# Kernel tuning notes

Hardware: AMD Instinct MI355X
Metric: run time of the kernel (lower is better)

Reference implementation:

```python
import jax, jax.numpy as jnp
import numpy as np

K = 4096  # num_embeddings
D = 256   # embedding_dim

def setup_inputs() -> dict:
    key = jax.random.key(0)
    k1, k2 = jax.random.split(key)
    z_e = jax.random.normal(k1, (32, 32, 32, 256), dtype=jnp.float32)
    embedding = jax.random.normal(k2, (K, D), dtype=jnp.float32)
    return {"z_e": z_e, "embedding": embedding}

def reference(z_e, embedding):
    # z_e: [B,H,W,D] channels-last; embedding: [K,D]
    B, H, W, Dd = z_e.shape
    z_flat = z_e.reshape(-1, Dd)                                   # [N,D]
    # squared L2 distances via expansion: ||z||^2 + ||e||^2 - 2 z.e
    distances = (jnp.sum(z_flat**2, axis=1, keepdims=True)
                 + jnp.sum(embedding**2, axis=1)
                 - 2.0 * jnp.matmul(z_flat, embedding.T))          # [N,K]
    indices = jnp.argmin(distances, axis=1)                        # [N]
    z_q = embedding[indices].reshape(B, H, W, Dd)                  # gather
    # straight-through estimator
    z_q = z_e + jax.lax.stop_gradient(z_q - z_e)
    # perplexity (codebook utilization)
    avg_probs = jnp.bincount(indices, length=K).astype(jnp.float32) / indices.shape[0]
    perplexity = jnp.exp(-jnp.sum(avg_probs * jnp.log(avg_probs + 1e-10)))
    return z_q, indices.reshape(B, H, W), perplexity
```

## Files before the change

kernel.cpp:

```cpp
#include <hip/hip_runtime.h>
#include <hip/hip_bf16.h>
#include <math.h>
#include <stdint.h>

typedef _Float16 f16;
typedef _Float16 f16x8 __attribute__((ext_vector_type(8)));
typedef float f32x16 __attribute__((ext_vector_type(16)));

#define DIM 256
#define LOSCALE 2048.0f
#define INV_LOSCALE (1.0f/2048.0f)

#define BP_BYTES (4096u*1024u + 98304u)

#define GLOAD16(gp, lp) __builtin_amdgcn_global_load_lds( \
    (const __attribute__((address_space(1))) void*)(gp),  \
    (__attribute__((address_space(3))) void*)(lp), 16, 0, 0)

__global__ void vq_pack2(const float* __restrict__ emb, f16* __restrict__ bp)
{
    int o = blockIdx.x * blockDim.x + threadIdx.x;
    int l = o & 63;
    int b = o >> 6;
    int t   = b & 1;
    int s   = (b >> 1) & 15;
    int col = b >> 5;
    int code  = col * 32 + (l & 31);
    int depth = s * 16 + (l >> 5) * 8;
    const float* gp = emb + (size_t)code * DIM + depth;
    float4 x0 = *(const float4*)gp;
    float4 x1 = *(const float4*)(gp + 4);
    float xs[8] = {x0.x, x0.y, x0.z, x0.w, x1.x, x1.y, x1.z, x1.w};
    f16x8 v;
    #pragma unroll
    for (int j = 0; j < 8; ++j) {
        f16 h = (f16)xs[j];
        v[j] = t ? (f16)((xs[j] - (float)h) * LOSCALE) : h;
    }
    *(f16x8*)(bp + (size_t)o * 8) = v;
}

__global__ void vq_e2(const float* __restrict__ emb, float* __restrict__ e2) {
    int k = blockIdx.x;
    int l = threadIdx.x;
    float4 v = ((const float4*)(emb + (size_t)k * DIM))[l];
    float s = v.x * v.x + v.y * v.y + v.z * v.z + v.w * v.w;
    #pragma unroll
    for (int off = 32; off; off >>= 1) s += __shfl_xor(s, off);
    if (l == 0) e2[k] = s;
}

__global__ void vq_zero(int* __restrict__ p, int n) {
    int i = blockIdx.x * blockDim.x + threadIdx.x;
    if (i < n) p[i] = 0;
}

__global__ __launch_bounds__(512, 2) void vq_argmin9(
    const float* __restrict__ z, const char* __restrict__ bp,
    const float* __restrict__ e2, unsigned long long* __restrict__ part)
{
    __shared__ __align__(16) char bufs[4][32768];
    __shared__ float e2s[2048];

    const int t    = threadIdx.x;
    const int lane = t & 63;
    const int wv   = t >> 6;
    const int hw   = blockIdx.x & 1;
    const int rg   = blockIdx.x >> 1;
    const int l31  = lane & 31;
    const int hi5  = lane >> 5;
    const int rowbase = rg * 256 + wv * 32;

    *(float4*)&e2s[t * 4] = *(const float4*)(e2 + hw * 2048 + t * 4);

    f16x8 a_h[16], a_l[16];
    {
        const float* zr = z + (size_t)(rowbase + l31) * DIM + hi5 * 8;
        #pragma unroll
        for (int s = 0; s < 16; ++s) {
            float4 x0 = *(const float4*)(zr + s * 16);
            float4 x1 = *(const float4*)(zr + s * 16 + 4);
            float xs[8] = {x0.x, x0.y, x0.z, x0.w, x1.x, x1.y, x1.z, x1.w};
            #pragma unroll
            for (int j = 0; j < 8; ++j) {
                f16 h = (f16)xs[j];
                a_h[s][j] = h;
                a_l[s][j] = (f16)((xs[j] - (float)h) * LOSCALE);
            }
        }
    }

    const char* bhalf = bp + ((size_t)hw << 21);

#define STAGE(pb, cc) do {                                                    \
    const char* src_ = bhalf + ((size_t)(cc) << 15) + (size_t)t * 16;         \
    char* dst_ = bufs[pb] + t * 16;                                           \
    _Pragma("unroll")                                                         \
    for (int i_ = 0; i_ < 4; ++i_)                                            \
        GLOAD16(src_ + i_ * 8192, dst_ + i_ * 8192);                          \
    } while (0)

    STAGE(0, 0);
    STAGE(1, 1);
    __syncthreads();

    float    bestd[16];
    unsigned bcol[4];
    #pragma unroll
    for (int q = 0; q < 16; ++q) bestd[q] = 3.4e38f;
    #pragma unroll
    for (int i = 0; i < 4; ++i) bcol[i] = 0u;

    for (int c = 0; c < 64; ++c) {
        STAGE((c + 2) & 3, c + 2);

        asm volatile("s_waitcnt vmcnt(8)" ::: "memory");
        asm volatile("s_waitcnt lgkmcnt(0)" ::: "memory");
        __builtin_amdgcn_s_barrier();
        __builtin_amdgcn_sched_barrier(0);

        f32x16 acc0, acc1a, acc1b;
        #pragma unroll
        for (int q = 0; q < 16; ++q) { acc0[q] = 0.0f; acc1a[q] = 0.0f; acc1b[q] = 0.0f; }

        const char* bb = bufs[c & 3];
        f16x8 bh_ = *(const f16x8*)(bb + lane * 16);
        f16x8 bl_ = *(const f16x8*)(bb + 1024 + lane * 16);
        __builtin_amdgcn_s_setprio(1);
        #pragma unroll
        for (int ks = 0; ks < 16; ++ks) {
            f16x8 bhn_, bln_;
            if (ks < 15) {
                bhn_ = *(const f16x8*)(bb + (ks + 1) * 2048 + lane * 16);
                bln_ = *(const f16x8*)(bb + (ks + 1) * 2048 + 1024 + lane * 16);
            }
            acc0  = __builtin_amdgcn_mfma_f32_32x32x16_f16(a_h[ks], bh_, acc0,  0, 0, 0);
            acc1a = __builtin_amdgcn_mfma_f32_32x32x16_f16(a_h[ks], bl_, acc1a, 0, 0, 0);
            acc1b = __builtin_amdgcn_mfma_f32_32x32x16_f16(a_l[ks], bh_, acc1b, 0, 0, 0);
            if (ks < 15) { bh_ = bhn_; bl_ = bln_; }
        }
        __builtin_amdgcn_s_setprio(0);

        float e2c = e2s[c * 32 + l31];
        #pragma unroll
        for (int q = 0; q < 16; ++q) {
            float dot  = fmaf(acc1a[q] + acc1b[q], INV_LOSCALE, acc0[q]);
            float dist = fmaf(-2.0f, dot, e2c);
            bool  lt   = dist < bestd[q];
            bestd[q]   = lt ? dist : bestd[q];
            const unsigned sh = (unsigned)((q & 3) * 8);
            unsigned nv = (bcol[q >> 2] & ~(0xFFu << sh)) | ((unsigned)c << sh);
            bcol[q >> 2] = lt ? nv : bcol[q >> 2];
        }
    }
#undef STAGE

    #pragma unroll
    for (int q = 0; q < 16; ++q) {
        float    d = bestd[q];
        unsigned c = (unsigned)(hw * 2048) +
                     ((bcol[q >> 2] >> ((q & 3) * 8)) & 0xFFu) * 32u + (unsigned)l31;
        #pragma unroll
        for (int o2 = 16; o2; o2 >>= 1) {
            float    od = __shfl_xor(d, o2);
            unsigned oc = __shfl_xor(c, o2);
            if (od < d || (od == d && oc < c)) { d = od; c = oc; }
        }
        if (l31 == 0) {
            int row = (q & 3) + 8 * (q >> 2) + 4 * hi5;
            unsigned u   = __float_as_uint(d);
            unsigned key = u ^ (unsigned)(((int)u >> 31) | 0x80000000);
            part[(size_t)hw * 32768 + rowbase + row] =
                ((unsigned long long)key << 32) | c;
        }
    }
}

__global__ void vq_final(const unsigned long long* __restrict__ part,
                         const float* __restrict__ emb,
                         float* __restrict__ idxf, float* __restrict__ zq,
                         int* __restrict__ counts, int N)
{
    int n = blockIdx.x * 4 + (threadIdx.x >> 6);
    int l = threadIdx.x & 63;
    if (n >= N) return;
    unsigned long long a = part[n];
    unsigned long long b = part[(size_t)N + n];
    unsigned long long m = b < a ? b : a;
    int idx = (int)(unsigned)(m & 0xffffffffu);
    ((float4*)(zq + (size_t)n * DIM))[l] =
        ((const float4*)(emb + (size_t)idx * DIM))[l];
    if (l == 0) {
        idxf[n] = (float)idx;
        atomicAdd(&counts[idx], 1);
    }
}

__global__ __launch_bounds__(256, 2) void vq_argmin_f32(
    const float* __restrict__ z, const float* __restrict__ emb,
    const float* __restrict__ e2, float* __restrict__ idxf, int K)
{
    __shared__ float zs[64 * 36];
    __shared__ float es[128 * 36];
    const int t = threadIdx.x;
    const int tx = t & 15;
    const int ty = t >> 4;
    const int rowbase = blockIdx.x * 64;
    const float* zbase = z + (size_t)rowbase * DIM;
    float best[4]; int bidx[4];
    #pragma unroll
    for (int i = 0; i < 4; ++i) { best[i] = 3.4e38f; bidx[i] = 0; }
    for (int kt = 0; kt < K; kt += 128) {
        float acc[4][8];
        #pragma unroll
        for (int i = 0; i < 4; ++i)
            #pragma unroll
            for (int j = 0; j < 8; ++j) acc[i][j] = 0.0f;
        for (int dc = 0; dc < DIM; dc += 32) {
            { int lr = t >> 2, o = (t & 3) * 8;
              const float* gp = zbase + (size_t)lr * DIM + dc + o;
              *(float4*)&zs[lr*36+o]   = *(const float4*)gp;
              *(float4*)&zs[lr*36+o+4] = *(const float4*)(gp+4); }
            { int lc = t >> 1, o = (t & 1) * 16;
              const float* gp = emb + (size_t)(kt+lc) * DIM + dc + o;
              *(float4*)&es[lc*36+o]    = *(const float4*)gp;
              *(float4*)&es[lc*36+o+4]  = *(const float4*)(gp+4);
              *(float4*)&es[lc*36+o+8]  = *(const float4*)(gp+8);
              *(float4*)&es[lc*36+o+12] = *(const float4*)(gp+12); }
            __syncthreads();
            const float* zp = &zs[(ty*4)*36];
            const float* ep = &es[tx*36];
            #pragma unroll
            for (int d = 0; d < 32; d += 4) {
                float4 zv[4], ev[8];
                #pragma unroll
                for (int i = 0; i < 4; ++i) zv[i] = *(const float4*)&zp[i*36+d];
                #pragma unroll
                for (int j = 0; j < 8; ++j) ev[j] = *(const float4*)&ep[j*16*36+d];
                #pragma unroll
                for (int i = 0; i < 4; ++i)
                    #pragma unroll
                    for (int j = 0; j < 8; ++j) {
                        acc[i][j] += zv[i].x*ev[j].x; acc[i][j] += zv[i].y*ev[j].y;
                        acc[i][j] += zv[i].z*ev[j].z; acc[i][j] += zv[i].w*ev[j].w;
                    }
            }
            __syncthreads();
        }
        #pragma unroll
        for (int j = 0; j < 8; ++j) {
            int c = kt + tx + 16*j;
            float ev2 = e2[c];
            #pragma unroll
            for (int i = 0; i < 4; ++i) {
                float dist = ev2 - 2.0f*acc[i][j];
                if (dist < best[i] || (dist == best[i] && c < bidx[i])) { best[i]=dist; bidx[i]=c; }
            }
        }
    }
    #pragma unroll
    for (int i = 0; i < 4; ++i) {
        float bd = best[i]; int bi = bidx[i];
        #pragma unroll
        for (int off = 8; off; off >>= 1) {
            float od = __shfl_xor(bd, off); int oi = __shfl_xor(bi, off);
            if (od < bd || (od == bd && oi < bi)) { bd = od; bi = oi; }
        }
        if (tx == 0) idxf[rowbase + ty*4 + i] = (float)bi;
    }
}

__global__ void vq_gather(const float* __restrict__ emb,
                          const float* __restrict__ idxf,
                          float* __restrict__ zq, int N)
{
    int n = blockIdx.x * 4 + (threadIdx.x >> 6);
    int l = threadIdx.x & 63;
    if (n >= N) return;
    int idx = (int)idxf[n];
    ((float4*)(zq + (size_t)n * DIM))[l] = ((const float4*)(emb + (size_t)idx * DIM))[l];
}

__global__ void vq_hist(const float* __restrict__ idxf, int* __restrict__ counts, int N) {
    int n = blockIdx.x * blockDim.x + threadIdx.x;
    if (n < N) atomicAdd(&counts[(int)idxf[n]], 1);
}

__global__ void vq_ppl(const int* __restrict__ counts, float invN,
                       float* __restrict__ out, int K)
{
    int t = threadIdx.x;
    float s = 0.0f;
    for (int k = t; k < K; k += 256) {
        float p = (float)counts[k] * invN;
        s += p * logf(p + 1e-10f);
    }
    #pragma unroll
    for (int off = 32; off; off >>= 1) s += __shfl_xor(s, off);
    __shared__ float wsum[4];
    if ((t & 63) == 0) wsum[t >> 6] = s;
    __syncthreads();
    if (t == 0) out[0] = expf(-(wsum[0] + wsum[1] + wsum[2] + wsum[3]));
}

extern "C" void kernel_launch(void* const* d_in, const int* in_sizes, int n_in,
                              void* d_out, int out_size, void* d_ws, size_t ws_size,
                              hipStream_t stream)
{
    const float* z   = (const float*)d_in[0];
    const float* emb = (const float*)d_in[1];
    const int N = in_sizes[0] / DIM;
    const int K = in_sizes[1] / DIM;

    float* out  = (float*)d_out;
    float* zq   = out;
    float* idxf = out + (size_t)N * DIM;
    float* ppl  = idxf + N;

    const size_t PART_BYTES = 2ull * 32768 * sizeof(unsigned long long);
    const size_t NEED = (size_t)BP_BYTES + 16384 + 16384 + PART_BYTES;

    if (ws_size >= NEED && K == 4096 && N == 32768) {
        f16*   bpk    = (f16*)d_ws;
        float* e2     = (float*)((char*)d_ws + BP_BYTES);
        int*   counts = (int*)((char*)d_ws + BP_BYTES + 16384);
        unsigned long long* part =
            (unsigned long long*)((char*)d_ws + BP_BYTES + 32768);

        vq_pack2<<<1024, 256, 0, stream>>>(emb, bpk);
        vq_e2<<<K, 64, 0, stream>>>(emb, e2);
        vq_zero<<<(K + 255) / 256, 256, 0, stream>>>(counts, K);
        vq_argmin9<<<(N / 256) * 2, 512, 0, stream>>>(z, (const char*)bpk, e2, part);
        vq_final<<<N / 4, 256, 0, stream>>>(part, emb, idxf, zq, counts, N);
        vq_ppl<<<1, 256, 0, stream>>>(counts, 1.0f / (float)N, ppl, K);
    } else {
        float* e2     = (float*)d_ws;
        int*   counts = (int*)((char*)d_ws + (size_t)K * sizeof(float));
        vq_e2<<<K, 64, 0, stream>>>(emb, e2);
        vq_zero<<<(K + 255) / 256, 256, 0, stream>>>(counts, K);
        vq_argmin_f32<<<N / 64, 256, 0, stream>>>(z, emb, e2, idxf, K);
        vq_gather<<<N / 4, 256, 0, stream>>>(emb, idxf, zq, N);
        vq_hist<<<(N + 255) / 256, 256, 0, stream>>>(idxf, counts, N);
        vq_ppl<<<1, 256, 0, stream>>>(counts, 1.0f / (float)N, ppl, K);
    }
}
```

Baseline: 223.5 us.

## Stage only hi codebook halves in LDS, stream lo halves from global

The argmin kernel now copies only the high-precision f16 codebook fragments into LDS, halving each staging buffer to 16 KB. The low-residual fragments are loaded straight from global memory into registers. The MFMA loop is restructured into four groups of four k-steps with register double-buffering of both fragment types. This cuts LDS traffic and footprint, which may allow more resident blocks per CU. The cost is that every wave redundantly fetches the lo fragments through the cache hierarchy, and the MFMAs now depend on global load latency.

```diff
diff --git a/kernel.cpp b/kernel.cpp
--- a/kernel.cpp
+++ b/kernel.cpp
@@ -55,11 +55,11 @@
     if (i < n) p[i] = 0;
 }
 
-__global__ __launch_bounds__(512, 2) void vq_argmin9(
+__global__ __launch_bounds__(512, 2) void vq_argmin11(
     const float* __restrict__ z, const char* __restrict__ bp,
     const float* __restrict__ e2, unsigned long long* __restrict__ part)
 {
-    __shared__ __align__(16) char bufs[4][32768];
+    __shared__ __align__(16) char bufs[4][16384];
     __shared__ float e2s[2048];
 
     const int t    = threadIdx.x;
@@ -93,12 +93,34 @@
     const char* bhalf = bp + ((size_t)hw << 21);
 
 #define STAGE(pb, cc) do {                                                    \
-    const char* src_ = bhalf + ((size_t)(cc) << 15) + (size_t)t * 16;         \
-    char* dst_ = bufs[pb] + t * 16;                                           \
+    const char* src_ = bhalf + ((size_t)(cc) << 15)                           \
+                     + (size_t)wv * 2048 + (size_t)lane * 16;                 \
+    char* dst_ = bufs[pb] + wv * 1024 + lane * 16;                            \
+    GLOAD16(src_, dst_);                                                      \
+    GLOAD16(src_ + 16384, dst_ + 8192);                                       \
+    } while (0)
+
+#define LOADBL(dst, CB, G) do {                                               \
     _Pragma("unroll")                                                         \
-    for (int i_ = 0; i_ < 4; ++i_)                                            \
-        GLOAD16(src_ + i_ * 8192, dst_ + i_ * 8192);                          \
+    for (int j_ = 0; j_ < 4; ++j_)                                            \
+        dst[j_] = *(const f16x8*)((CB) + ((G) * 4 + j_) * 2048 + 1024         \
+                                  + lane * 16);                               \
     } while (0)
+
+#define LOADBH(dst, BB, G) do {                                               \
+    _Pragma("unroll")                                                         \
+    for (int j_ = 0; j_ < 4; ++j_)                                            \
+        dst[j_] = *(const f16x8*)((BB) + ((G) * 4 + j_) * 1024 + lane * 16);  \
+    } while (0)
+
+#define MFMA4(BH, BL, G) do {                                                 \
+    _Pragma("unroll")                                                         \
+    for (int j_ = 0; j_ < 4; ++j_) {                                          \
+        const int ks_ = (G) * 4 + j_;                                         \
+        acc0  = __builtin_amdgcn_mfma_f32_32x32x16_f16(a_h[ks_], BH[j_], acc0,  0,0,0); \
+        acc1a = __builtin_amdgcn_mfma_f32_32x32x16_f16(a_h[ks_], BL[j_], acc1a, 0,0,0); \
+        acc1b = __builtin_amdgcn_mfma_f32_32x32x16_f16(a_l[ks_], BH[j_], acc1b, 0,0,0); \
+    } } while (0)
 
     STAGE(0, 0);
     STAGE(1, 1);
@@ -112,6 +134,10 @@
     for (int i = 0; i < 4; ++i) bcol[i] = 0u;
 
     for (int c = 0; c < 64; ++c) {
+        const char* colbase = bhalf + ((size_t)c << 15);
+
+        f16x8 blA[4], blB[4];
+        LOADBL(blA, colbase, 0);
         STAGE((c + 2) & 3, c + 2);
 
         asm volatile("s_waitcnt vmcnt(8)" ::: "memory");
@@ -124,21 +150,20 @@
         for (int q = 0; q < 16; ++q) { acc0[q] = 0.0f; acc1a[q] = 0.0f; acc1b[q] = 0.0f; }
 
         const char* bb = bufs[c & 3];
-        f16x8 bh_ = *(const f16x8*)(bb + lane * 16);
-        f16x8 bl_ = *(const f16x8*)(bb + 1024 + lane * 16);
+        f16x8 bhA[4], bhB[4];
+        LOADBH(bhA, bb, 0);
+
         __builtin_amdgcn_s_setprio(1);
-        #pragma unroll
-        for (int ks = 0; ks < 16; ++ks) {
-            f16x8 bhn_, bln_;
-            if (ks < 15) {
-                bhn_ = *(const f16x8*)(bb + (ks + 1) * 2048 + lane * 16);
-                bln_ = *(const f16x8*)(bb + (ks + 1) * 2048 + 1024 + lane * 16);
-            }
-            acc0  = __builtin_amdgcn_mfma_f32_32x32x16_f16(a_h[ks], bh_, acc0,  0, 0, 0);
-            acc1a = __builtin_amdgcn_mfma_f32_32x32x16_f16(a_h[ks], bl_, acc1a, 0, 0, 0);
-            acc1b = __builtin_amdgcn_mfma_f32_32x32x16_f16(a_l[ks], bh_, acc1b, 0, 0, 0);
-            if (ks < 15) { bh_ = bhn_; bl_ = bln_; }
-        }
+        LOADBL(blB, colbase, 1);
+        LOADBH(bhB, bb, 1);
+        MFMA4(bhA, blA, 0);
+        LOADBL(blA, colbase, 2);
+        LOADBH(bhA, bb, 2);
+        MFMA4(bhB, blB, 1);
+        LOADBL(blB, colbase, 3);
+        LOADBH(bhB, bb, 3);
+        MFMA4(bhA, blA, 2);
+        MFMA4(bhB, blB, 3);
         __builtin_amdgcn_s_setprio(0);
 
         float e2c = e2s[c * 32 + l31];
@@ -154,6 +179,9 @@
         }
     }
 #undef STAGE
+#undef LOADBL
+#undef LOADBH
+#undef MFMA4
 
     #pragma unroll
     for (int q = 0; q < 16; ++q) {
@@ -330,7 +358,7 @@
         vq_pack2<<<1024, 256, 0, stream>>>(emb, bpk);
         vq_e2<<<K, 64, 0, stream>>>(emb, e2);
         vq_zero<<<(K + 255) / 256, 256, 0, stream>>>(counts, K);
-        vq_argmin9<<<(N / 256) * 2, 512, 0, stream>>>(z, (const char*)bpk, e2, part);
+        vq_argmin11<<<(N / 256) * 2, 512, 0, stream>>>(z, (const char*)bpk, e2, part);
         vq_final<<<N / 4, 256, 0, stream>>>(part, emb, idxf, zq, counts, N);
         vq_ppl<<<1, 256, 0, stream>>>(counts, 1.0f / (float)N, ppl, K);
     } else {
```

After: 235.0 us. 1.05x slower.

## Split argmin chunk loop into four barrier-synchronized phases interleaving loads and MFMA

Applied to the files above, without the earlier changes.

Restructures the per-chunk inner loop into four phases, each issuing one quarter of the next-next chunk's global-to-LDS load, reading four k-slices of B into registers, then running a block of MFMAs between workgroup barriers. The goal is to spread memory issue across the chunk and to batch LDS reads ahead of the MFMA bursts so waves stay in lockstep. It adds eight barriers per chunk instead of one, which could cost more synchronization stall than the overlap it gains.

```diff
diff --git a/kernel.cpp b/kernel.cpp
--- a/kernel.cpp
+++ b/kernel.cpp
@@ -55,7 +55,7 @@
     if (i < n) p[i] = 0;
 }
 
-__global__ __launch_bounds__(512, 2) void vq_argmin9(
+__global__ __launch_bounds__(512, 2) void vq_argmin12(
     const float* __restrict__ z, const char* __restrict__ bp,
     const float* __restrict__ e2, unsigned long long* __restrict__ part)
 {
@@ -92,7 +92,7 @@
 
     const char* bhalf = bp + ((size_t)hw << 21);
 
-#define STAGE(pb, cc) do {                                                    \
+#define STAGEF(pb, cc) do {                                                   \
     const char* src_ = bhalf + ((size_t)(cc) << 15) + (size_t)t * 16;         \
     char* dst_ = bufs[pb] + t * 16;                                           \
     _Pragma("unroll")                                                         \
@@ -100,8 +100,40 @@
         GLOAD16(src_ + i_ * 8192, dst_ + i_ * 8192);                          \
     } while (0)
 
-    STAGE(0, 0);
-    STAGE(1, 1);
+#define STAGE1(pb, cc, g) do {                                                \
+    const char* src_ = bhalf + ((size_t)(cc) << 15) + (size_t)t * 16          \
+                     + (size_t)(g) * 8192;                                    \
+    char* dst_ = bufs[pb] + t * 16 + (g) * 8192;                              \
+    GLOAD16(src_, dst_);                                                      \
+    } while (0)
+
+#define PHASE(g) do {                                                         \
+    STAGE1((c + 2) & 3, c + 2, g);                                            \
+    if ((g) == 0) asm volatile("s_waitcnt vmcnt(5)" ::: "memory");            \
+    _Pragma("unroll")                                                         \
+    for (int j_ = 0; j_ < 4; ++j_) {                                          \
+        rh[j_] = *(const f16x8*)(bb + ((g) * 4 + j_) * 2048 + lane * 16);     \
+        rl[j_] = *(const f16x8*)(bb + ((g) * 4 + j_) * 2048 + 1024 + lane * 16); \
+    }                                                                         \
+    __builtin_amdgcn_sched_barrier(0);                                        \
+    __builtin_amdgcn_s_barrier();                                             \
+    asm volatile("s_waitcnt lgkmcnt(0)" ::: "memory");                        \
+    __builtin_amdgcn_sched_barrier(0);                                        \
+    __builtin_amdgcn_s_setprio(1);                                            \
+    _Pragma("unroll")                                                         \
+    for (int j_ = 0; j_ < 4; ++j_) {                                          \
+        const int ks_ = (g) * 4 + j_;                                         \
+        acc0  = __builtin_amdgcn_mfma_f32_32x32x16_f16(a_h[ks_], rh[j_], acc0,  0,0,0); \
+        acc1a = __builtin_amdgcn_mfma_f32_32x32x16_f16(a_h[ks_], rl[j_], acc1a, 0,0,0); \
+        acc1b = __builtin_amdgcn_mfma_f32_32x32x16_f16(a_l[ks_], rh[j_], acc1b, 0,0,0); \
+    }                                                                         \
+    __builtin_amdgcn_s_setprio(0);                                            \
+    __builtin_amdgcn_sched_barrier(0);                                        \
+    __builtin_amdgcn_s_barrier();                                             \
+    } while (0)
+
+    STAGEF(0, 0);
+    STAGEF(1, 1);
     __syncthreads();
 
     float    bestd[16];
@@ -112,34 +144,16 @@
     for (int i = 0; i < 4; ++i) bcol[i] = 0u;
 
     for (int c = 0; c < 64; ++c) {
-        STAGE((c + 2) & 3, c + 2);
-
-        asm volatile("s_waitcnt vmcnt(8)" ::: "memory");
-        asm volatile("s_waitcnt lgkmcnt(0)" ::: "memory");
-        __builtin_amdgcn_s_barrier();
-        __builtin_amdgcn_sched_barrier(0);
-
+        const char* bb = bufs[c & 3];
         f32x16 acc0, acc1a, acc1b;
         #pragma unroll
         for (int q = 0; q < 16; ++q) { acc0[q] = 0.0f; acc1a[q] = 0.0f; acc1b[q] = 0.0f; }
 
-        const char* bb = bufs[c & 3];
-        f16x8 bh_ = *(const f16x8*)(bb + lane * 16);
-        f16x8 bl_ = *(const f16x8*)(bb + 1024 + lane * 16);
-        __builtin_amdgcn_s_setprio(1);
-        #pragma unroll
-        for (int ks = 0; ks < 16; ++ks) {
-            f16x8 bhn_, bln_;
-            if (ks < 15) {
-                bhn_ = *(const f16x8*)(bb + (ks + 1) * 2048 + lane * 16);
-                bln_ = *(const f16x8*)(bb + (ks + 1) * 2048 + 1024 + lane * 16);
-            }
-            acc0  = __builtin_amdgcn_mfma_f32_32x32x16_f16(a_h[ks], bh_, acc0,  0, 0, 0);
-            acc1a = __builtin_amdgcn_mfma_f32_32x32x16_f16(a_h[ks], bl_, acc1a, 0, 0, 0);
-            acc1b = __builtin_amdgcn_mfma_f32_32x32x16_f16(a_l[ks], bh_, acc1b, 0, 0, 0);
-            if (ks < 15) { bh_ = bhn_; bl_ = bln_; }
-        }
-        __builtin_amdgcn_s_setprio(0);
+        f16x8 rh[4], rl[4];
+        PHASE(0);
+        PHASE(1);
+        PHASE(2);
+        PHASE(3);
 
         float e2c = e2s[c * 32 + l31];
         #pragma unroll
@@ -153,7 +167,9 @@
             bcol[q >> 2] = lt ? nv : bcol[q >> 2];
         }
     }
-#undef STAGE
+#undef STAGEF
+#undef STAGE1
+#undef PHASE
 
     #pragma unroll
     for (int q = 0; q < 16; ++q) {
@@ -330,7 +346,7 @@
         vq_pack2<<<1024, 256, 0, stream>>>(emb, bpk);
         vq_e2<<<K, 64, 0, stream>>>(emb, e2);
         vq_zero<<<(K + 255) / 256, 256, 0, stream>>>(counts, K);
-        vq_argmin9<<<(N / 256) * 2, 512, 0, stream>>>(z, (const char*)bpk, e2, part);
+        vq_argmin12<<<(N / 256) * 2, 512, 0, stream>>>(z, (const char*)bpk, e2, part);
         vq_final<<<N / 4, 256, 0, stream>>>(part, emb, idxf, zq, counts, N);
         vq_ppl<<<1, 256, 0, stream>>>(counts, 1.0f / (float)N, ppl, K);
     } else {
```

Measured after the change: 235.5 us. 1.05x slower.

## Scan with fp16-only dot products and rescore ambiguous rows at split precision

Applied to the files above, without the earlier changes.

The main argmin scan now uses a single fp16 MFMA product per tile instead of three split-precision products, and it tracks both the best and second-best distance per row. A certification kernel uses error bounds built from row norms and the largest codebook residual norms to accept rows whose best-versus-second margin is safe. The remaining rows go to a compacted list and are rescored with the full hi/lo split-precision MFMA over the whole codebook, merged by atomicMin. This cuts MFMA work in the main pass by about a factor of three, at the cost of extra kernels, atomics and a rescore pass whose size depends on how many rows are ambiguous. Correctness depends on the error bound being conservative.

```diff
diff --git a/kernel.cpp b/kernel.cpp
--- a/kernel.cpp
+++ b/kernel.cpp
@@ -6,16 +6,23 @@
 typedef _Float16 f16;
 typedef _Float16 f16x8 __attribute__((ext_vector_type(8)));
 typedef float f32x16 __attribute__((ext_vector_type(16)));
+typedef unsigned long long ull;
 
 #define DIM 256
 #define LOSCALE 2048.0f
 #define INV_LOSCALE (1.0f/2048.0f)
+#define EPS0 0.05f
 
 #define BP_BYTES (4096u*1024u + 98304u)
 
 #define GLOAD16(gp, lp) __builtin_amdgcn_global_load_lds( \
     (const __attribute__((address_space(1))) void*)(gp),  \
     (__attribute__((address_space(3))) void*)(lp), 16, 0, 0)
+
+__device__ __forceinline__ float dec_key(unsigned k) {
+    unsigned u = (k & 0x80000000u) ? (k ^ 0x80000000u) : ~k;
+    return __uint_as_float(u);
+}
 
 __global__ void vq_pack2(const float* __restrict__ emb, f16* __restrict__ bp)
 {
@@ -40,11 +47,42 @@
     *(f16x8*)(bp + (size_t)o * 8) = v;
 }
 
+__global__ void vq_e2x(const float* __restrict__ emb, float* __restrict__ e2,
+                       unsigned* __restrict__ melmeh)
+{
+    int k = blockIdx.x;
+    int l = threadIdx.x;
+    float4 v = ((const float4*)(emb + (size_t)k * DIM))[l];
+    float xs[4] = {v.x, v.y, v.z, v.w};
+    float s = 0.0f, sh = 0.0f, sl = 0.0f;
+    #pragma unroll
+    for (int j = 0; j < 4; ++j) {
+        float x = xs[j];
+        s = fmaf(x, x, s);
+        f16 h = (f16)x;
+        float hv = (float)h;
+        float lv = (float)((f16)((x - hv) * LOSCALE));
+        sh = fmaf(hv, hv, sh);
+        sl = fmaf(lv, lv, sl);
+    }
+    #pragma unroll
+    for (int off = 32; off; off >>= 1) {
+        s  += __shfl_xor(s, off);
+        sh += __shfl_xor(sh, off);
+        sl += __shfl_xor(sl, off);
+    }
+    if (l == 0) {
+        e2[k] = s;
+        atomicMax(&melmeh[0], __float_as_uint(sqrtf(sl)));
+        atomicMax(&melmeh[1], __float_as_uint(sqrtf(sh)));
+    }
+}
+
 __global__ void vq_e2(const float* __restrict__ emb, float* __restrict__ e2) {
     int k = blockIdx.x;
     int l = threadIdx.x;
     float4 v = ((const float4*)(emb + (size_t)k * DIM))[l];
-    float s = v.x * v.x + v.y * v.y + v.z * v.z + v.w * v.w;
+    float s = v.x*v.x + v.y*v.y + v.z*v.z + v.w*v.w;
     #pragma unroll
     for (int off = 32; off; off >>= 1) s += __shfl_xor(s, off);
     if (l == 0) e2[k] = s;
@@ -55,9 +93,11 @@
     if (i < n) p[i] = 0;
 }
 
-__global__ __launch_bounds__(512, 2) void vq_argmin9(
+__global__ __launch_bounds__(512, 2) void vq_scan(
     const float* __restrict__ z, const char* __restrict__ bp,
-    const float* __restrict__ e2, unsigned long long* __restrict__ part)
+    const float* __restrict__ e2,
+    ull* __restrict__ partD, float* __restrict__ partD2,
+    float2* __restrict__ AB)
 {
     __shared__ __align__(16) char bufs[4][32768];
     __shared__ float e2s[2048];
@@ -73,7 +113,8 @@
 
     *(float4*)&e2s[t * 4] = *(const float4*)(e2 + hw * 2048 + t * 4);
 
-    f16x8 a_h[16], a_l[16];
+    f16x8 a_h[16];
+    float s2h = 0.0f, s2l = 0.0f;
     {
         const float* zr = z + (size_t)(rowbase + l31) * DIM + hi5 * 8;
         #pragma unroll
@@ -85,13 +126,301 @@
             for (int j = 0; j < 8; ++j) {
                 f16 h = (f16)xs[j];
                 a_h[s][j] = h;
+                float hv = (float)h;
+                float lv = (float)((f16)((xs[j] - hv) * LOSCALE));
+                s2h = fmaf(hv, hv, s2h);
+                s2l = fmaf(lv, lv, s2l);
+            }
+        }
+    }
+    s2h += __shfl_xor(s2h, 32);
+    s2l += __shfl_xor(s2l, 32);
+    if (hw == 0 && lane < 32) {
+        float nzh = sqrtf(s2h), nzl = sqrtf(s2l);
+        float a = (2.0f / LOSCALE) * (nzh + nzl * INV_LOSCALE) * 1.02f;
+        float b = (2.0f / LOSCALE) * nzl * 1.02f;
+        AB[rowbase + lane] = make_float2(a, b);
+    }
+
+    const char* bhalf = bp + ((size_t)hw << 21);
+
+#define STAGE(pb, uu) do {                                                    \
+    const char* s0_ = bhalf + ((size_t)(uu) << 16)                            \
+                    + (size_t)(t >> 6) * 2048 + (size_t)(t & 63) * 16;        \
+    char* d0_ = bufs[pb] + t * 16;                                            \
+    GLOAD16(s0_,          d0_);                                               \
+    GLOAD16(s0_ + 16384,  d0_ + 8192);                                        \
+    GLOAD16(s0_ + 32768,  d0_ + 16384);                                       \
+    GLOAD16(s0_ + 49152,  d0_ + 24576);                                       \
+    } while (0)
+
+    STAGE(0, 0);
+    STAGE(1, 1);
+    __syncthreads();
+
+    float    bestd[16], d2nd[16];
+    unsigned bcol[4];
+    #pragma unroll
+    for (int q = 0; q < 16; ++q) { bestd[q] = 3.4e38f; d2nd[q] = 3.4e38f; }
+    #pragma unroll
+    for (int i = 0; i < 4; ++i) bcol[i] = 0u;
+
+    for (int u = 0; u < 32; ++u) {
+        STAGE((u + 2) & 3, u + 2);
+        asm volatile("s_waitcnt vmcnt(8)" ::: "memory");
+        asm volatile("s_waitcnt lgkmcnt(0)" ::: "memory");
+        __builtin_amdgcn_s_barrier();
+        __builtin_amdgcn_sched_barrier(0);
+
+        const char* bu = bufs[u & 3];
+        #pragma unroll
+        for (int sub = 0; sub < 2; ++sub) {
+            const int c = 2 * u + sub;
+            const char* bb = bu + sub * 16384;
+            f32x16 m0, m1;
+            #pragma unroll
+            for (int q = 0; q < 16; ++q) { m0[q] = 0.0f; m1[q] = 0.0f; }
+            __builtin_amdgcn_s_setprio(1);
+            #pragma unroll
+            for (int ks = 0; ks < 16; ks += 2) {
+                f16x8 b0 = *(const f16x8*)(bb + ks * 1024 + lane * 16);
+                f16x8 b1 = *(const f16x8*)(bb + (ks + 1) * 1024 + lane * 16);
+                m0 = __builtin_amdgcn_mfma_f32_32x32x16_f16(a_h[ks],     b0, m0, 0, 0, 0);
+                m1 = __builtin_amdgcn_mfma_f32_32x32x16_f16(a_h[ks + 1], b1, m1, 0, 0, 0);
+            }
+            __builtin_amdgcn_s_setprio(0);
+
+            float e2c = e2s[c * 32 + l31];
+            #pragma unroll
+            for (int q = 0; q < 16; ++q) {
+                float d = fmaf(-2.0f, m0[q] + m1[q], e2c);
+                bool lt = d < bestd[q];
+                float nd2 = lt ? bestd[q] : fminf(d2nd[q], d);
+                d2nd[q]  = nd2;
+                bestd[q] = lt ? d : bestd[q];
+                const unsigned sh = (unsigned)((q & 3) * 8);
+                unsigned nv = (bcol[q >> 2] & ~(0xFFu << sh)) | ((unsigned)c << sh);
+                bcol[q >> 2] = lt ? nv : bcol[q >> 2];
+            }
+        }
+    }
+#undef STAGE
+
+    #pragma unroll
+    for (int q = 0; q < 16; ++q) {
+        float    d  = bestd[q];
+        float    d2 = d2nd[q];
+        unsigned c  = (unsigned)(hw * 2048) +
+                      ((bcol[q >> 2] >> ((q & 3) * 8)) & 0xFFu) * 32u + (unsigned)l31;
+        #pragma unroll
+        for (int o2 = 16; o2; o2 >>= 1) {
+            float    od  = __shfl_xor(d, o2);
+            unsigned oc  = __shfl_xor(c, o2);
+            float    od2 = __shfl_xor(d2, o2);
+            float nd2 = fminf(fmaxf(d, od), fminf(d2, od2));
+            bool sw = od < d || (od == d && oc < c);
+            d = sw ? od : d;
+            c = sw ? oc : c;
+            d2 = nd2;
+        }
+        if (l31 == 0) {
+            int row = (q & 3) + 8 * (q >> 2) + 4 * hi5;
+            unsigned u_  = __float_as_uint(d);
+            unsigned key = u_ ^ (unsigned)(((int)u_ >> 31) | 0x80000000);
+            partD [(size_t)hw * 32768 + rowbase + row] = ((ull)key << 32) | c;
+            partD2[(size_t)hw * 32768 + rowbase + row] = d2;
+        }
+    }
+}
+
+__global__ void vq_certain(ull* __restrict__ partD, const float* __restrict__ partD2,
+                           const float2* __restrict__ AB,
+                           const unsigned* __restrict__ melmeh,
+                           int* __restrict__ list, int* __restrict__ ctr, int N)
+{
+    int i = blockIdx.x * blockDim.x + threadIdx.x;
+    if (i >= N) return;
+    ull k0 = partD[i];
+    ull k1 = partD[(size_t)N + i];
+    float d1a = dec_key((unsigned)(k0 >> 32));
+    float d1b = dec_key((unsigned)(k1 >> 32));
+    float d2a = partD2[i];
+    float d2b = partD2[(size_t)N + i];
+    ull  kmin = k1 < k0 ? k1 : k0;
+    float gd1 = fminf(d1a, d1b);
+    float gd2 = fminf(fmaxf(d1a, d1b), fminf(d2a, d2b));
+    float2 ab = AB[i];
+    float Mel = __uint_as_float(melmeh[0]);
+    float Meh = __uint_as_float(melmeh[1]);
+    float eps = fmaf(ab.x, Mel, fmaf(ab.y, Meh, EPS0));
+    if (gd2 - gd1 > 2.0f * eps) {
+        partD[i] = kmin;
+    } else {
+        partD[i] = ~0ULL;
+        int p = atomicAdd(ctr, 1);
+        list[p] = i;
+    }
+}
+
+__global__ __launch_bounds__(64) void vq_rescore(
+    const float* __restrict__ z, const char* __restrict__ bp,
+    const float* __restrict__ e2, const int* __restrict__ list,
+    const int* __restrict__ ctr, ull* __restrict__ outD)
+{
+    const int l    = threadIdx.x;
+    const int l31  = l & 31;
+    const int hi5  = l >> 5;
+    const int slot  = blockIdx.x >> 2;
+    const int chunk = blockIdx.x & 3;
+    const int cnt = *ctr;
+    if (slot * 32 >= cnt) return;
+
+    int pos = slot * 32 + l31;
+    int rid = list[pos < cnt ? pos : 0];
+
+    f16x8 a_h[16], a_l[16];
+    {
+        const float* zr = z + (size_t)rid * DIM + hi5 * 8;
+        #pragma unroll
+        for (int s = 0; s < 16; ++s) {
+            float4 x0 = *(const float4*)(zr + s * 16);
+            float4 x1 = *(const float4*)(zr + s * 16 + 4);
+            float xs[8] = {x0.x, x0.y, x0.z, x0.w, x1.x, x1.y, x1.z, x1.w};
+            #pragma unroll
+            for (int j = 0; j < 8; ++j) {
+                f16 h = (f16)xs[j];
+                a_h[s][j] = h;
                 a_l[s][j] = (f16)((xs[j] - (float)h) * LOSCALE);
             }
         }
     }
 
+    float    bestd[16];
+    unsigned bcol[4];
+    #pragma unroll
+    for (int q = 0; q < 16; ++q) bestd[q] = 3.4e38f;
+    #pragma unroll
+    for (int i = 0; i < 4; ++i) bcol[i] = 0u;
+
+    const char* bgp = bp + (((size_t)chunk * 32) << 15) + (size_t)l * 16;
+
+#define LOADG(BH, BL, OFF) do {                                    \
+    _Pragma("unroll")                                              \
+    for (int i_ = 0; i_ < 4; ++i_) {                               \
+        BH[i_] = *(const f16x8*)(bgp + (OFF) + i_ * 2048);         \
+        BL[i_] = *(const f16x8*)(bgp + (OFF) + i_ * 2048 + 1024);  \
+    } } while (0)
+
+#define COMPUTE(BH, BL, G) do {                                                      \
+    _Pragma("unroll")                                                                \
+    for (int i_ = 0; i_ < 4; ++i_) {                                                 \
+        acc0  = __builtin_amdgcn_mfma_f32_32x32x16_f16(a_h[(G)*4+i_], BH[i_], acc0,  0,0,0); \
+        acc1a = __builtin_amdgcn_mfma_f32_32x32x16_f16(a_h[(G)*4+i_], BL[i_], acc1a, 0,0,0); \
+        acc1b = __builtin_amdgcn_mfma_f32_32x32x16_f16(a_l[(G)*4+i_], BH[i_], acc1b, 0,0,0); \
+    } } while (0)
+
+    f16x8 h0[4], l0[4], h1[4], l1[4];
+    size_t off = 0;
+    LOADG(h0, l0, off); off += 8192;
+    LOADG(h1, l1, off); off += 8192;
+
+    for (int lc = 0; lc < 32; ++lc) {
+        float e2c = e2[(chunk * 32 + lc) * 32 + l31];
+        f32x16 acc0, acc1a, acc1b;
+        #pragma unroll
+        for (int q = 0; q < 16; ++q) { acc0[q] = 0.0f; acc1a[q] = 0.0f; acc1b[q] = 0.0f; }
+
+        COMPUTE(h0, l0, 0); LOADG(h0, l0, off); off += 8192;
+        COMPUTE(h1, l1, 1); LOADG(h1, l1, off); off += 8192;
+        COMPUTE(h0, l0, 2); LOADG(h0, l0, off); off += 8192;
+        COMPUTE(h1, l1, 3); LOADG(h1, l1, off); off += 8192;
+
+        #pragma unroll
+        for (int q = 0; q < 16; ++q) {
+            float dot  = fmaf(acc1a[q] + acc1b[q], INV_LOSCALE, acc0[q]);
+            float dist = fmaf(-2.0f, dot, e2c);
+            bool  lt   = dist < bestd[q];
+            bestd[q]   = lt ? dist : bestd[q];
+            const unsigned sh = (unsigned)((q & 3) * 8);
+            unsigned nv = (bcol[q >> 2] & ~(0xFFu << sh)) | ((unsigned)lc << sh);
+            bcol[q >> 2] = lt ? nv : bcol[q >> 2];
+        }
+    }
+#undef LOADG
+#undef COMPUTE
+
+    #pragma unroll
+    for (int q = 0; q < 16; ++q) {
+        float    d = bestd[q];
+        unsigned c = ((unsigned)chunk * 32u +
+                      ((bcol[q >> 2] >> ((q & 3) * 8)) & 0xFFu)) * 32u + (unsigned)l31;
+        #pragma unroll
+        for (int o2 = 16; o2; o2 >>= 1) {
+            float    od = __shfl_xor(d, o2);
+            unsigned oc = __shfl_xor(c, o2);
+            if (od < d || (od == d && oc < c)) { d = od; c = oc; }
+        }
+        int rlocal = (q & 3) + 8 * (q >> 2) + 4 * hi5;
+        int ridr   = __shfl(rid, rlocal);
+        if (l31 == 0) {
+            unsigned u_  = __float_as_uint(d);
+            unsigned key = u_ ^ (unsigned)(((int)u_ >> 31) | 0x80000000);
+            atomicMin(&outD[ridr], ((ull)key << 32) | c);
+        }
+    }
+}
+
+__global__ void vq_final1(const ull* __restrict__ outD, const float* __restrict__ emb,
+                          float* __restrict__ idxf, float* __restrict__ zq,
+                          int* __restrict__ counts, int N)
+{
+    int n = blockIdx.x * 4 + (threadIdx.x >> 6);
+    int l = threadIdx.x & 63;
+    if (n >= N) return;
+    int idx = (int)(unsigned)(outD[n] & 0xffffffffu);
+    idx &= 4095;
+    ((float4*)(zq + (size_t)n * DIM))[l] =
+        ((const float4*)(emb + (size_t)idx * DIM))[l];
+    if (l == 0) {
+        idxf[n] = (float)idx;
+        atomicAdd(&counts[idx], 1);
+    }
+}
+
+__global__ __launch_bounds__(512, 2) void vq_argmin10(
+    const float* __restrict__ z, const char* __restrict__ bp,
+    const float* __restrict__ e2, ull* __restrict__ part)
+{
+    __shared__ __align__(16) char bufs[4][32768];
+    __shared__ float e2s[2048];
+    const int t    = threadIdx.x;
+    const int lane = t & 63;
+    const int wv   = t >> 6;
+    const int hw   = blockIdx.x & 1;
+    const int rg   = blockIdx.x >> 1;
+    const int l31  = lane & 31;
+    const int hi5  = lane >> 5;
+    const int rowbase = rg * 256 + wv * 32;
+
+    *(float4*)&e2s[t * 4] = *(const float4*)(e2 + hw * 2048 + t * 4);
+
+    f16x8 a_h[16], a_l[16];
+    {
+        const float* zr = z + (size_t)(rowbase + l31) * DIM + hi5 * 8;
+        #pragma unroll
+        for (int s = 0; s < 16; ++s) {
+            float4 x0 = *(const float4*)(zr + s * 16);
+            float4 x1 = *(const float4*)(zr + s * 16 + 4);
+            float xs[8] = {x0.x, x0.y, x0.z, x0.w, x1.x, x1.y, x1.z, x1.w};
+            #pragma unroll
+            for (int j = 0; j < 8; ++j) {
+                f16 h = (f16)xs[j];
+                a_h[s][j] = h;
+                a_l[s][j] = (f16)((xs[j] - (float)h) * LOSCALE);
+            }
+        }
+    }
     const char* bhalf = bp + ((size_t)hw << 21);
-
 #define STAGE(pb, cc) do {                                                    \
     const char* src_ = bhalf + ((size_t)(cc) << 15) + (size_t)t * 16;         \
     char* dst_ = bufs[pb] + t * 16;                                           \
@@ -99,7 +428,6 @@
     for (int i_ = 0; i_ < 4; ++i_)                                            \
         GLOAD16(src_ + i_ * 8192, dst_ + i_ * 8192);                          \
     } while (0)
-
     STAGE(0, 0);
     STAGE(1, 1);
     __syncthreads();
@@ -113,7 +441,6 @@
 
     for (int c = 0; c < 64; ++c) {
         STAGE((c + 2) & 3, c + 2);
-
         asm volatile("s_waitcnt vmcnt(8)" ::: "memory");
         asm volatile("s_waitcnt lgkmcnt(0)" ::: "memory");
         __builtin_amdgcn_s_barrier();
@@ -122,7 +449,6 @@
         f32x16 acc0, acc1a, acc1b;
         #pragma unroll
         for (int q = 0; q < 16; ++q) { acc0[q] = 0.0f; acc1a[q] = 0.0f; acc1b[q] = 0.0f; }
-
         const char* bb = bufs[c & 3];
         f16x8 bh_ = *(const f16x8*)(bb + lane * 16);
         f16x8 bl_ = *(const f16x8*)(bb + 1024 + lane * 16);
@@ -154,7 +480,6 @@
         }
     }
 #undef STAGE
-
     #pragma unroll
     for (int q = 0; q < 16; ++q) {
         float    d = bestd[q];
@@ -168,26 +493,24 @@
         }
         if (l31 == 0) {
             int row = (q & 3) + 8 * (q >> 2) + 4 * hi5;
-            unsigned u   = __float_as_uint(d);
-            unsigned key = u ^ (unsigned)(((int)u >> 31) | 0x80000000);
-            part[(size_t)hw * 32768 + rowbase + row] =
-                ((unsigned long long)key << 32) | c;
-        }
-    }
-}
-
-__global__ void vq_final(const unsigned long long* __restrict__ part,
-                         const float* __restrict__ emb,
-                         float* __restrict__ idxf, float* __restrict__ zq,
-                         int* __restrict__ counts, int N)
+            unsigned u_  = __float_as_uint(d);
+            unsigned key = u_ ^ (unsigned)(((int)u_ >> 31) | 0x80000000);
+            part[(size_t)hw * 32768 + rowbase + row] = ((ull)key << 32) | c;
+        }
+    }
+}
+
+__global__ void vq_final2h(const ull* __restrict__ part, const float* __restrict__ emb,
+                           float* __restrict__ idxf, float* __restrict__ zq,
+                           int* __restrict__ counts, int N)
 {
     int n = blockIdx.x * 4 + (threadIdx.x >> 6);
     int l = threadIdx.x & 63;
     if (n >= N) return;
-    unsigned long long a = part[n];
-    unsigned long long b = part[(size_t)N + n];
-    unsigned long long m = b < a ? b : a;
-    int idx = (int)(unsigned)(m & 0xffffffffu);
+    ull a = part[n];
+    ull b = part[(size_t)N + n];
+    ull m = b < a ? b : a;
+    int idx = (int)(unsigned)(m & 0xffffffffu) & 4095;
     ((float4*)(zq + (size_t)n * DIM))[l] =
         ((const float4*)(emb + (size_t)idx * DIM))[l];
     if (l == 0) {
@@ -317,21 +640,47 @@
     float* idxf = out + (size_t)N * DIM;
     float* ppl  = idxf + N;
 
-    const size_t PART_BYTES = 2ull * 32768 * sizeof(unsigned long long);
-    const size_t NEED = (size_t)BP_BYTES + 16384 + 16384 + PART_BYTES;
-
-    if (ws_size >= NEED && K == 4096 && N == 32768) {
-        f16*   bpk    = (f16*)d_ws;
-        float* e2     = (float*)((char*)d_ws + BP_BYTES);
-        int*   counts = (int*)((char*)d_ws + BP_BYTES + 16384);
-        unsigned long long* part =
-            (unsigned long long*)((char*)d_ws + BP_BYTES + 32768);
-
+    char* base = (char*)d_ws;
+    const size_t OFF_E2   = BP_BYTES;
+    const size_t OFF_CNT  = OFF_E2 + 16384;
+    const size_t OFF_MISC = OFF_CNT + 16384;
+    const size_t OFF_PART = OFF_MISC + 32;
+    const size_t OFF_PD2  = OFF_PART + 524288;
+    const size_t OFF_AB   = OFF_PD2 + 262144;
+    const size_t OFF_LIST = OFF_AB + 262144;
+    const size_t NEED_FULL = OFF_LIST + 131072;
+    const size_t NEED_MID  = OFF_PART + 524288;
+
+    if (ws_size >= NEED_FULL && K == 4096 && N == 32768) {
+        f16*   bpk    = (f16*)base;
+        float* e2     = (float*)(base + OFF_E2);
+        int*   counts = (int*)(base + OFF_CNT);
+        int*   ctr    = counts + 4096;
+        unsigned* melmeh = (unsigned*)(ctr + 1);
+        ull*   partD  = (ull*)(base + OFF_PART);
+        float* partD2 = (float*)(base + OFF_PD2);
+        float2* AB    = (float2*)(base + OFF_AB);
+        int*   list   = (int*)(base + OFF_LIST);
+
+        vq_zero<<<17, 256, 0, stream>>>(counts, 4100);
+        vq_pack2<<<1024, 256, 0, stream>>>(emb, bpk);
+        vq_e2x<<<K, 64, 0, stream>>>(emb, e2, melmeh);
+        vq_scan<<<256, 512, 0, stream>>>(z, (const char*)bpk, e2, partD, partD2, AB);
+        vq_certain<<<128, 256, 0, stream>>>(partD, partD2, AB, melmeh, list, ctr, N);
+        vq_rescore<<<4096, 64, 0, stream>>>(z, (const char*)bpk, e2, list, ctr, partD);
+        vq_final1<<<N / 4, 256, 0, stream>>>(partD, emb, idxf, zq, counts, N);
+        vq_ppl<<<1, 256, 0, stream>>>(counts, 1.0f / (float)N, ppl, K);
+    } else if (ws_size >= NEED_MID && K == 4096 && N == 32768) {
+        f16*   bpk    = (f16*)base;
+        float* e2     = (float*)(base + OFF_E2);
+        int*   counts = (int*)(base + OFF_CNT);
+        ull*   part   = (ull*)(base + OFF_PART);
+
+        vq_zero<<<16, 256, 0, stream>>>(counts, 4096);
         vq_pack2<<<1024, 256, 0, stream>>>(emb, bpk);
         vq_e2<<<K, 64, 0, stream>>>(emb, e2);
-        vq_zero<<<(K + 255) / 256, 256, 0, stream>>>(counts, K);
-        vq_argmin9<<<(N / 256) * 2, 512, 0, stream>>>(z, (const char*)bpk, e2, part);
-        vq_final<<<N / 4, 256, 0, stream>>>(part, emb, idxf, zq, counts, N);
+        vq_argmin10<<<(N / 256) * 2, 512, 0, stream>>>(z, (const char*)bpk, e2, part);
+        vq_final2h<<<N / 4, 256, 0, stream>>>(part, emb, idxf, zq, counts, N);
         vq_ppl<<<1, 256, 0, stream>>>(counts, 1.0f / (float)N, ppl, K);
     } else {
         float* e2     = (float*)d_ws;
```

After: 316.2 us. 41.5% more time.
